# Kernel tuning notes

Hardware: AMD Instinct MI355X
Metric: run time of the kernel (lower is better)

## Reference

```python
import jax, jax.numpy as jnp
import numpy as np

KM_ITERS = 20  # fixed Lloyd iterations (scipy kmeans iterates to tolerance with random init;
               # we use deterministic min/max init so centroid 0 = dark, 1 = bright)


def _kmeans_mask(img2d):
    """2-means clustering of pixel intensities of one [H,W] image + border-vote flip."""
    H, W = img2d.shape
    x = img2d.reshape(-1)  # [N]
    c0 = jnp.stack([x.min(), x.max()])  # deterministic init: centroid0=min, centroid1=max

    def step(c, _):
        code = jnp.argmin(jnp.abs(x[:, None] - c[None, :]), axis=1)  # [N] in {0,1}
        one = code == 1
        n1 = jnp.sum(one)
        n0 = x.shape[0] - n1
        s1 = jnp.sum(jnp.where(one, x, jnp.zeros_like(x)))
        s0 = jnp.sum(x) - s1
        c_new = jnp.stack([s0 / jnp.maximum(n0, 1).astype(x.dtype),
                           s1 / jnp.maximum(n1, 1).astype(x.dtype)])
        return c_new, None

    c, _ = jax.lax.scan(step, c0, None, length=KM_ITERS)
    # final assignment (scipy vq step)
    code = jnp.argmin(jnp.abs(x[:, None] - c[None, :]), axis=1).reshape(H, W)

    # border vote: if >=3 borders are mostly cluster-1, flip so text region is 1
    fc = code[:, 0].sum()
    lc = code[:, -1].sum()
    fr = code[0, :].sum()
    lr = code[-1, :].sum()
    num = ((fr > W // 2).astype(jnp.int32) + (lr > W // 2).astype(jnp.int32)
           + (fc > H // 2).astype(jnp.int32) + (lc > H // 2).astype(jnp.int32))
    mask = jnp.where(num >= 3, 1 - code, code)
    return mask.astype(img2d.dtype)


def get_mask(img_tensor):
    gray = img_tensor.mean(axis=1)  # [B,H,W]
    # clustering is non-differentiable in the original (runs on detached CPU numpy)
    masks = jax.vmap(_kmeans_mask)(jax.lax.stop_gradient(gray))
    return masks[:, None, :, :]  # [B,1,H,W]


def setup_inputs() -> dict:
    key = jax.random.key(0)
    k1, k2 = jax.random.split(key)
    B, C, H, W = 128, 3, 256, 256
    hr_img = jax.random.uniform(k1, (B, C, H, W), dtype=jnp.float32)
    sr_mask = jax.random.uniform(k2, (B, 1, H, W), dtype=jnp.float32)
    return {"hr_img": hr_img, "sr_mask": sr_mask}


def reference(hr_img, sr_mask):
    hr_mask = get_mask(hr_img)  # same spatial size -> no interpolation branch
    return jnp.mean((sr_mask - hr_mask) ** 2)
```

## Files before the change

kernel.cpp:

```cpp
#include <hip/hip_runtime.h>


constexpr int TPB  = 1024;
constexpr int NW   = TPB / 64;
constexpr int NPIX = 65536;
constexpr int VPT  = NPIX / TPB;
constexpr int V4   = VPT / 4;
constexpr int KM_ITERS = 20;

__device__ __forceinline__ float waveSum(float v) {
#pragma unroll
    for (int off = 32; off > 0; off >>= 1) v += __shfl_down(v, off, 64);
    return v;
}
__device__ __forceinline__ float waveMin(float v) {
#pragma unroll
    for (int off = 32; off > 0; off >>= 1) v = fminf(v, __shfl_down(v, off, 64));
    return v;
}
__device__ __forceinline__ float waveMax(float v) {
#pragma unroll
    for (int off = 32; off > 0; off >>= 1) v = fmaxf(v, __shfl_down(v, off, 64));
    return v;
}

__global__ __launch_bounds__(TPB) void kmeans_mask_loss(
        const float* __restrict__ hr, const float* __restrict__ sr,
        float* __restrict__ ws) {
    const int img  = blockIdx.x;
    const int tid  = threadIdx.x;
    const int lane = tid & 63;
    const int wid  = tid >> 6;

    __shared__ float4 sm4[NW];
    __shared__ float  bc[4];

    const float* r = hr + (size_t)img * 3 * NPIX;
    const float* g = r + NPIX;
    const float* b = g + NPIX;

    float v[VPT];
#pragma unroll
    for (int i = 0; i < V4; ++i) {
        const int p = 4 * tid + 4096 * i;
        float4 rr = *(const float4*)(r + p);
        float4 gg = *(const float4*)(g + p);
        float4 bb = *(const float4*)(b + p);
        v[4*i+0] = (rr.x + gg.x + bb.x) * (1.0f / 3.0f);
        v[4*i+1] = (rr.y + gg.y + bb.y) * (1.0f / 3.0f);
        v[4*i+2] = (rr.z + gg.z + bb.z) * (1.0f / 3.0f);
        v[4*i+3] = (rr.w + gg.w + bb.w) * (1.0f / 3.0f);
    }

    float mn = v[0], mx = v[0], sm = 0.0f;
#pragma unroll
    for (int i = 0; i < VPT; ++i) {
        mn = fminf(mn, v[i]); mx = fmaxf(mx, v[i]); sm += v[i];
    }
    mn = waveMin(mn); mx = waveMax(mx); sm = waveSum(sm);
    if (lane == 0) sm4[wid] = make_float4(mn, mx, sm, 0.0f);
    __syncthreads();
    if (wid == 0) {
        float4 x = (lane < NW) ? sm4[lane] : make_float4(3.0e38f, -3.0e38f, 0.0f, 0.0f);
        x.x = waveMin(x.x); x.y = waveMax(x.y); x.z = waveSum(x.z);
        if (lane == 0) { bc[0] = x.x; bc[1] = x.y; bc[2] = x.z; }
    }
    __syncthreads();
    float c0 = bc[0], c1 = bc[1];
    const float S = bc[2];

#pragma unroll 1
    for (int it = 0; it < KM_ITERS; ++it) {
        const float t = 0.5f * (c0 + c1);
        float s1 = 0.0f, n1 = 0.0f;
        if (c1 >= c0) {
#pragma unroll
            for (int i = 0; i < VPT; ++i)
                if (v[i] > t) { s1 += v[i]; n1 += 1.0f; }
        } else {
#pragma unroll
            for (int i = 0; i < VPT; ++i)
                if (v[i] < t) { s1 += v[i]; n1 += 1.0f; }
        }
        s1 = waveSum(s1); n1 = waveSum(n1);
        if (lane == 0) sm4[wid] = make_float4(s1, n1, 0.0f, 0.0f);
        __syncthreads();
        if (wid == 0) {
            float4 x = (lane < NW) ? sm4[lane] : make_float4(0.0f, 0.0f, 0.0f, 0.0f);
            x.x = waveSum(x.x); x.y = waveSum(x.y);
            if (lane == 0) {
                const float S1 = x.x, N1 = x.y;
                bc[1] = S1 / fmaxf(N1, 1.0f);
                bc[0] = (S - S1) / fmaxf((float)NPIX - N1, 1.0f);
            }
        }
        __syncthreads();
        const float nc0 = bc[0], nc1 = bc[1];
        const bool conv = (nc0 == c0) && (nc1 == c1);
        c0 = nc0; c1 = nc1;
        if (conv) break;
    }

    const float t  = 0.5f * (c0 + c1);
    const bool  hi = (c1 >= c0);
    float fc = 0.0f, lc = 0.0f, fr = 0.0f, lr = 0.0f;
#pragma unroll
    for (int i = 0; i < V4; ++i) {
#pragma unroll
        for (int j = 0; j < 4; ++j) {
            const int p   = 4 * tid + 4096 * i + j;
            const int col = p & 255;
            const int row = p >> 8;
            const bool code = hi ? (v[4*i+j] > t) : (v[4*i+j] < t);
            const float cf = code ? 1.0f : 0.0f;
            if (col == 0)   fc += cf;
            if (col == 255) lc += cf;
            if (row == 0)   fr += cf;
            if (row == 255) lr += cf;
        }
    }
    fc = waveSum(fc); lc = waveSum(lc); fr = waveSum(fr); lr = waveSum(lr);
    if (lane == 0) sm4[wid] = make_float4(fc, lc, fr, lr);
    __syncthreads();
    if (wid == 0) {
        float4 x = (lane < NW) ? sm4[lane] : make_float4(0.0f, 0.0f, 0.0f, 0.0f);
        x.x = waveSum(x.x); x.y = waveSum(x.y); x.z = waveSum(x.z); x.w = waveSum(x.w);
        if (lane == 0) {
            const int num = (x.z > 128.0f) + (x.w > 128.0f) +
                            (x.x > 128.0f) + (x.y > 128.0f);
            bc[0] = (num >= 3) ? 1.0f : 0.0f;
        }
    }
    __syncthreads();
    const bool flip = (bc[0] != 0.0f);

    const float* srp = sr + (size_t)img * NPIX;
    float acc = 0.0f;
#pragma unroll
    for (int i = 0; i < V4; ++i) {
        const int p = 4 * tid + 4096 * i;
        float4 s = *(const float4*)(srp + p);
#pragma unroll
        for (int j = 0; j < 4; ++j) {
            const bool code = hi ? (v[4*i+j] > t) : (v[4*i+j] < t);
            const float m = (code != flip) ? 1.0f : 0.0f;
            const float sv = (j == 0) ? s.x : (j == 1) ? s.y : (j == 2) ? s.z : s.w;
            const float d = sv - m;
            acc += d * d;
        }
    }
    acc = waveSum(acc);
    if (lane == 0) sm4[wid] = make_float4(acc, 0.0f, 0.0f, 0.0f);
    __syncthreads();
    if (wid == 0) {
        float x = (lane < NW) ? sm4[lane].x : 0.0f;
        x = waveSum(x);
        if (lane == 0) ws[img] = x;
    }
}

__global__ void finalize_kernel(const float* __restrict__ ws, float* __restrict__ out) {
    const int lane = threadIdx.x;
    float v = ws[lane] + ws[lane + 64];
    v = waveSum(v);
    if (lane == 0) out[0] = v * (1.0f / 8388608.0f);
}

extern "C" void kernel_launch(void* const* d_in, const int* in_sizes, int n_in,
                              void* d_out, int out_size, void* d_ws, size_t ws_size,
                              hipStream_t stream) {
    const float* hr = (const float*)d_in[0];
    const float* sr = (const float*)d_in[1];
    float* out = (float*)d_out;
    float* ws  = (float*)d_ws;

    kmeans_mask_loss<<<128, TPB, 0, stream>>>(hr, sr, ws);
    finalize_kernel<<<1, 64, 0, stream>>>(ws, out);
}
```

Measured before the change: 218.7 us.

## Replace per-pixel Lloyd iterations with histogram prefix-sum k-means across split kernels

The single-block-per-image kernel is replaced by a pipeline. First a 2048-bin per-image histogram of counts and sums is built across 8 blocks per image. One thread then runs the Lloyd iterations against prefix sums, interpolating linearly inside the threshold bin, and separate kernels handle the border vote and the MSE. This removes the 20 passes over register-resident pixels and the low occupancy of 128 blocks. In exchange it re-reads the image twice, adds a memset and five launches, and approximates the threshold-bin split, so centroids and masks can differ from the exact result.

```diff
diff --git a/kernel.cpp b/kernel.cpp
--- a/kernel.cpp
+++ b/kernel.cpp
@@ -1,12 +1,17 @@
 #include <hip/hip_runtime.h>
 
 
-constexpr int TPB  = 1024;
-constexpr int NW   = TPB / 64;
+constexpr int NB   = 2048;
 constexpr int NPIX = 65536;
-constexpr int VPT  = NPIX / TPB;
-constexpr int V4   = VPT / 4;
 constexpr int KM_ITERS = 20;
+
+constexpr size_t OFF_MINENC = 0;
+constexpr size_t OFF_MAXBIT = 512;
+constexpr size_t OFF_TINFO  = 1024;
+constexpr size_t OFF_HCNT   = 4096;
+constexpr size_t OFF_HSUM   = OFF_HCNT + (size_t)128 * NB * 4;
+constexpr size_t OFF_BSUM   = OFF_HSUM + (size_t)128 * NB * 4;
+constexpr size_t MEMSET_BYTES = OFF_BSUM;
 
 __device__ __forceinline__ float waveSum(float v) {
 #pragma unroll
@@ -24,146 +29,227 @@
     return v;
 }
 
-__global__ __launch_bounds__(TPB) void kmeans_mask_loss(
-        const float* __restrict__ hr, const float* __restrict__ sr,
-        float* __restrict__ ws) {
-    const int img  = blockIdx.x;
-    const int tid  = threadIdx.x;
-    const int lane = tid & 63;
-    const int wid  = tid >> 6;
-
-    __shared__ float4 sm4[NW];
-    __shared__ float  bc[4];
+__global__ __launch_bounds__(256) void kA_hist(
+        const float* __restrict__ hr, unsigned* __restrict__ minenc,
+        unsigned* __restrict__ maxbits, unsigned* __restrict__ hcnt,
+        float* __restrict__ hsum) {
+    const int img = blockIdx.x >> 3, part = blockIdx.x & 7, tid = threadIdx.x;
+    const int lane = tid & 63, wid = tid >> 6;
+
+    __shared__ unsigned hcL[NB];
+    __shared__ float    hsL[NB];
+    __shared__ float    smn[4], smx[4];
+    for (int j = tid; j < NB; j += 256) { hcL[j] = 0u; hsL[j] = 0.0f; }
+    __syncthreads();
 
     const float* r = hr + (size_t)img * 3 * NPIX;
     const float* g = r + NPIX;
     const float* b = g + NPIX;
 
-    float v[VPT];
-#pragma unroll
-    for (int i = 0; i < V4; ++i) {
-        const int p = 4 * tid + 4096 * i;
+    float mn = 1e30f, mx = -1e30f;
+#pragma unroll
+    for (int i = 0; i < 8; ++i) {
+        const int p = part * 8192 + i * 1024 + tid * 4;
         float4 rr = *(const float4*)(r + p);
         float4 gg = *(const float4*)(g + p);
         float4 bb = *(const float4*)(b + p);
-        v[4*i+0] = (rr.x + gg.x + bb.x) * (1.0f / 3.0f);
-        v[4*i+1] = (rr.y + gg.y + bb.y) * (1.0f / 3.0f);
-        v[4*i+2] = (rr.z + gg.z + bb.z) * (1.0f / 3.0f);
-        v[4*i+3] = (rr.w + gg.w + bb.w) * (1.0f / 3.0f);
-    }
-
-    float mn = v[0], mx = v[0], sm = 0.0f;
-#pragma unroll
-    for (int i = 0; i < VPT; ++i) {
-        mn = fminf(mn, v[i]); mx = fmaxf(mx, v[i]); sm += v[i];
-    }
-    mn = waveMin(mn); mx = waveMax(mx); sm = waveSum(sm);
-    if (lane == 0) sm4[wid] = make_float4(mn, mx, sm, 0.0f);
-    __syncthreads();
-    if (wid == 0) {
-        float4 x = (lane < NW) ? sm4[lane] : make_float4(3.0e38f, -3.0e38f, 0.0f, 0.0f);
-        x.x = waveMin(x.x); x.y = waveMax(x.y); x.z = waveSum(x.z);
-        if (lane == 0) { bc[0] = x.x; bc[1] = x.y; bc[2] = x.z; }
-    }
-    __syncthreads();
-    float c0 = bc[0], c1 = bc[1];
-    const float S = bc[2];
-
+        float x[4] = { (rr.x + gg.x + bb.x) * (1.0f / 3.0f),
+                       (rr.y + gg.y + bb.y) * (1.0f / 3.0f),
+                       (rr.z + gg.z + bb.z) * (1.0f / 3.0f),
+                       (rr.w + gg.w + bb.w) * (1.0f / 3.0f) };
+#pragma unroll
+        for (int j = 0; j < 4; ++j) {
+            mn = fminf(mn, x[j]); mx = fmaxf(mx, x[j]);
+            int k = (int)(x[j] * (float)NB);
+            k = max(0, min(NB - 1, k));
+            atomicAdd(&hcL[k], 1u);
+            atomicAdd(&hsL[k], x[j]);
+        }
+    }
+    __syncthreads();
+
+    for (int j = tid; j < NB; j += 256) {
+        unsigned c = hcL[j];
+        if (c) {
+            atomicAdd(&hcnt[(size_t)img * NB + j], c);
+            unsafeAtomicAdd(&hsum[(size_t)img * NB + j], hsL[j]);
+        }
+    }
+
+    mn = waveMin(mn); mx = waveMax(mx);
+    if (lane == 0) { smn[wid] = mn; smx[wid] = mx; }
+    __syncthreads();
+    if (tid == 0) {
+        float bmn = fminf(fminf(smn[0], smn[1]), fminf(smn[2], smn[3]));
+        float bmx = fmaxf(fmaxf(smx[0], smx[1]), fmaxf(smx[2], smx[3]));
+        atomicMax(&maxbits[img], __float_as_uint(bmx));
+        atomicMax(&minenc[img], 0xFFFFFFFFu - __float_as_uint(bmn));
+    }
+}
+
+__global__ __launch_bounds__(256) void kB_lloyd(
+        const unsigned* __restrict__ minenc, const unsigned* __restrict__ maxbits,
+        const unsigned* __restrict__ hcnt, const float* __restrict__ hsum,
+        float4* __restrict__ tinfo) {
+    const int img = blockIdx.x, tid = threadIdx.x;
+    __shared__ float sN[NB + 1], sS[NB + 1];
+    __shared__ float tN[256], tS[256];
+
+    const int base = tid * 8;
+    float n8[8], s8[8];
+#pragma unroll
+    for (int u = 0; u < 8; ++u) {
+        n8[u] = (float)hcnt[(size_t)img * NB + base + u];
+        s8[u] = hsum[(size_t)img * NB + base + u];
+    }
+    float accN = 0.0f, accS = 0.0f;
+#pragma unroll
+    for (int u = 7; u >= 0; --u) {
+        accN += n8[u]; n8[u] = accN;
+        accS += s8[u]; s8[u] = accS;
+    }
+    tN[tid] = accN; tS[tid] = accS;
+    __syncthreads();
+    for (int off = 1; off < 256; off <<= 1) {
+        float aN = 0.0f, aS = 0.0f;
+        if (tid + off < 256) { aN = tN[tid + off]; aS = tS[tid + off]; }
+        __syncthreads();
+        tN[tid] += aN; tS[tid] += aS;
+        __syncthreads();
+    }
+    const float exN = (tid < 255) ? tN[tid + 1] : 0.0f;
+    const float exS = (tid < 255) ? tS[tid + 1] : 0.0f;
+#pragma unroll
+    for (int u = 0; u < 8; ++u) { sN[base + u] = n8[u] + exN; sS[base + u] = s8[u] + exS; }
+    if (tid == 0) { sN[NB] = 0.0f; sS[NB] = 0.0f; }
+    __syncthreads();
+
+    if (tid == 0) {
+        const float mn = __uint_as_float(0xFFFFFFFFu - minenc[img]);
+        const float mx = __uint_as_float(maxbits[img]);
+        const float Stot = sS[0];
+        const float Ntot = (float)NPIX;
+        float c0 = mn, c1 = mx;
 #pragma unroll 1
-    for (int it = 0; it < KM_ITERS; ++it) {
-        const float t = 0.5f * (c0 + c1);
-        float s1 = 0.0f, n1 = 0.0f;
-        if (c1 >= c0) {
-#pragma unroll
-            for (int i = 0; i < VPT; ++i)
-                if (v[i] > t) { s1 += v[i]; n1 += 1.0f; }
-        } else {
-#pragma unroll
-            for (int i = 0; i < VPT; ++i)
-                if (v[i] < t) { s1 += v[i]; n1 += 1.0f; }
-        }
-        s1 = waveSum(s1); n1 = waveSum(n1);
-        if (lane == 0) sm4[wid] = make_float4(s1, n1, 0.0f, 0.0f);
-        __syncthreads();
-        if (wid == 0) {
-            float4 x = (lane < NW) ? sm4[lane] : make_float4(0.0f, 0.0f, 0.0f, 0.0f);
-            x.x = waveSum(x.x); x.y = waveSum(x.y);
-            if (lane == 0) {
-                const float S1 = x.x, N1 = x.y;
-                bc[1] = S1 / fmaxf(N1, 1.0f);
-                bc[0] = (S - S1) / fmaxf((float)NPIX - N1, 1.0f);
+        for (int it = 0; it < KM_ITERS; ++it) {
+            const float t = 0.5f * (c0 + c1);
+            float n1, s1;
+            if (c1 == c0) { n1 = 0.0f; s1 = 0.0f; }
+            else {
+                const float f = t * (float)NB;
+                int k = (int)floorf(f);
+                k = max(0, min(NB - 1, k));
+                float frac = (float)(k + 1) - f;
+                frac = fminf(fmaxf(frac, 0.0f), 1.0f);
+                const float cntk = sN[k] - sN[k + 1];
+                const float sumk = sS[k] - sS[k + 1];
+                const float aN = sN[k + 1] + cntk * frac;
+                const float aS = sS[k + 1] + sumk * frac;
+                if (c1 > c0) { n1 = aN; s1 = aS; }
+                else         { n1 = Ntot - aN; s1 = Stot - aS; }
             }
-        }
-        __syncthreads();
-        const float nc0 = bc[0], nc1 = bc[1];
-        const bool conv = (nc0 == c0) && (nc1 == c1);
-        c0 = nc0; c1 = nc1;
-        if (conv) break;
-    }
-
-    const float t  = 0.5f * (c0 + c1);
-    const bool  hi = (c1 >= c0);
-    float fc = 0.0f, lc = 0.0f, fr = 0.0f, lr = 0.0f;
-#pragma unroll
-    for (int i = 0; i < V4; ++i) {
+            const float c1n = s1 / fmaxf(n1, 1.0f);
+            const float c0n = (Stot - s1) / fmaxf(Ntot - n1, 1.0f);
+            if (c1n == c1 && c0n == c0) break;
+            c0 = c0n; c1 = c1n;
+        }
+        float tf, hii;
+        if (c1 == c0) { tf = -1e30f; hii = 0.0f; }
+        else { tf = 0.5f * (c0 + c1); hii = (c1 > c0) ? 1.0f : 0.0f; }
+        tinfo[img] = make_float4(tf, hii, 0.0f, 0.0f);
+    }
+}
+
+__global__ __launch_bounds__(256) void kC_border(
+        const float* __restrict__ hr, float4* __restrict__ tinfo) {
+    const int img = blockIdx.x, tid = threadIdx.x;
+    const int lane = tid & 63, wid = tid >> 6;
+    __shared__ float4 sm[4];
+
+    const float4 ti = tinfo[img];
+    const float t = ti.x;
+    const bool hi = (ti.y != 0.0f);
+
+    const float* r = hr + (size_t)img * 3 * NPIX;
+    const float* g = r + NPIX;
+    const float* b = g + NPIX;
+
+    auto codeAt = [&](int p) -> float {
+        const float x = (r[p] + g[p] + b[p]) * (1.0f / 3.0f);
+        const bool one = hi ? (x > t) : (x < t);
+        return one ? 1.0f : 0.0f;
+    };
+    float fr = codeAt(tid);
+    float lr = codeAt(255 * 256 + tid);
+    float fc = codeAt(tid * 256);
+    float lc = codeAt(tid * 256 + 255);
+
+    fr = waveSum(fr); lr = waveSum(lr); fc = waveSum(fc); lc = waveSum(lc);
+    if (lane == 0) sm[wid] = make_float4(fr, lr, fc, lc);
+    __syncthreads();
+    if (tid == 0) {
+        float FR = sm[0].x + sm[1].x + sm[2].x + sm[3].x;
+        float LR = sm[0].y + sm[1].y + sm[2].y + sm[3].y;
+        float FC = sm[0].z + sm[1].z + sm[2].z + sm[3].z;
+        float LC = sm[0].w + sm[1].w + sm[2].w + sm[3].w;
+        const int num = (FR > 128.0f) + (LR > 128.0f) + (FC > 128.0f) + (LC > 128.0f);
+        tinfo[img].z = (num >= 3) ? 1.0f : 0.0f;
+    }
+}
+
+__global__ __launch_bounds__(256) void kD_mse(
+        const float* __restrict__ hr, const float* __restrict__ sr,
+        const float4* __restrict__ tinfo, float* __restrict__ bsum) {
+    const int img = blockIdx.x >> 3, part = blockIdx.x & 7, tid = threadIdx.x;
+    const int lane = tid & 63, wid = tid >> 6;
+    __shared__ float sm[4];
+
+    const float4 ti = tinfo[img];
+    const float t = ti.x;
+    const bool hi   = (ti.y != 0.0f);
+    const bool flip = (ti.z != 0.0f);
+
+    const float* r = hr + (size_t)img * 3 * NPIX;
+    const float* g = r + NPIX;
+    const float* b = g + NPIX;
+    const float* s = sr + (size_t)img * NPIX;
+
+    float acc = 0.0f;
+#pragma unroll
+    for (int i = 0; i < 8; ++i) {
+        const int p = part * 8192 + i * 1024 + tid * 4;
+        float4 rr = *(const float4*)(r + p);
+        float4 gg = *(const float4*)(g + p);
+        float4 bb = *(const float4*)(b + p);
+        float4 ss = *(const float4*)(s + p);
+        float x[4] = { (rr.x + gg.x + bb.x) * (1.0f / 3.0f),
+                       (rr.y + gg.y + bb.y) * (1.0f / 3.0f),
+                       (rr.z + gg.z + bb.z) * (1.0f / 3.0f),
+                       (rr.w + gg.w + bb.w) * (1.0f / 3.0f) };
+        float sv[4] = { ss.x, ss.y, ss.z, ss.w };
 #pragma unroll
         for (int j = 0; j < 4; ++j) {
-            const int p   = 4 * tid + 4096 * i + j;
-            const int col = p & 255;
-            const int row = p >> 8;
-            const bool code = hi ? (v[4*i+j] > t) : (v[4*i+j] < t);
-            const float cf = code ? 1.0f : 0.0f;
-            if (col == 0)   fc += cf;
-            if (col == 255) lc += cf;
-            if (row == 0)   fr += cf;
-            if (row == 255) lr += cf;
-        }
-    }
-    fc = waveSum(fc); lc = waveSum(lc); fr = waveSum(fr); lr = waveSum(lr);
-    if (lane == 0) sm4[wid] = make_float4(fc, lc, fr, lr);
-    __syncthreads();
-    if (wid == 0) {
-        float4 x = (lane < NW) ? sm4[lane] : make_float4(0.0f, 0.0f, 0.0f, 0.0f);
-        x.x = waveSum(x.x); x.y = waveSum(x.y); x.z = waveSum(x.z); x.w = waveSum(x.w);
-        if (lane == 0) {
-            const int num = (x.z > 128.0f) + (x.w > 128.0f) +
-                            (x.x > 128.0f) + (x.y > 128.0f);
-            bc[0] = (num >= 3) ? 1.0f : 0.0f;
-        }
-    }
-    __syncthreads();
-    const bool flip = (bc[0] != 0.0f);
-
-    const float* srp = sr + (size_t)img * NPIX;
-    float acc = 0.0f;
-#pragma unroll
-    for (int i = 0; i < V4; ++i) {
-        const int p = 4 * tid + 4096 * i;
-        float4 s = *(const float4*)(srp + p);
-#pragma unroll
-        for (int j = 0; j < 4; ++j) {
-            const bool code = hi ? (v[4*i+j] > t) : (v[4*i+j] < t);
-            const float m = (code != flip) ? 1.0f : 0.0f;
-            const float sv = (j == 0) ? s.x : (j == 1) ? s.y : (j == 2) ? s.z : s.w;
-            const float d = sv - m;
+            const bool one = hi ? (x[j] > t) : (x[j] < t);
+            const float m = (one != flip) ? 1.0f : 0.0f;
+            const float d = sv[j] - m;
             acc += d * d;
         }
     }
     acc = waveSum(acc);
-    if (lane == 0) sm4[wid] = make_float4(acc, 0.0f, 0.0f, 0.0f);
-    __syncthreads();
-    if (wid == 0) {
-        float x = (lane < NW) ? sm4[lane].x : 0.0f;
-        x = waveSum(x);
-        if (lane == 0) ws[img] = x;
-    }
-}
-
-__global__ void finalize_kernel(const float* __restrict__ ws, float* __restrict__ out) {
-    const int lane = threadIdx.x;
-    float v = ws[lane] + ws[lane + 64];
+    if (lane == 0) sm[wid] = acc;
+    __syncthreads();
+    if (tid == 0) bsum[blockIdx.x] = sm[0] + sm[1] + sm[2] + sm[3];
+}
+
+__global__ __launch_bounds__(256) void kE_final(
+        const float* __restrict__ bsum, float* __restrict__ out) {
+    const int tid = threadIdx.x, lane = tid & 63, wid = tid >> 6;
+    __shared__ float sm[4];
+    float v = bsum[tid] + bsum[tid + 256] + bsum[tid + 512] + bsum[tid + 768];
     v = waveSum(v);
-    if (lane == 0) out[0] = v * (1.0f / 8388608.0f);
+    if (lane == 0) sm[wid] = v;
+    __syncthreads();
+    if (tid == 0) out[0] = (sm[0] + sm[1] + sm[2] + sm[3]) * (1.0f / 8388608.0f);
 }
 
 extern "C" void kernel_launch(void* const* d_in, const int* in_sizes, int n_in,
@@ -172,8 +258,19 @@
     const float* hr = (const float*)d_in[0];
     const float* sr = (const float*)d_in[1];
     float* out = (float*)d_out;
-    float* ws  = (float*)d_ws;
-
-    kmeans_mask_loss<<<128, TPB, 0, stream>>>(hr, sr, ws);
-    finalize_kernel<<<1, 64, 0, stream>>>(ws, out);
-}
+
+    char* ws = (char*)d_ws;
+    unsigned* minenc  = (unsigned*)(ws + OFF_MINENC);
+    unsigned* maxbits = (unsigned*)(ws + OFF_MAXBIT);
+    float4*   tinfo   = (float4*)(ws + OFF_TINFO);
+    unsigned* hcnt    = (unsigned*)(ws + OFF_HCNT);
+    float*    hsum    = (float*)(ws + OFF_HSUM);
+    float*    bsum    = (float*)(ws + OFF_BSUM);
+
+    hipMemsetAsync(d_ws, 0, MEMSET_BYTES, stream);
+    kA_hist  <<<1024, 256, 0, stream>>>(hr, minenc, maxbits, hcnt, hsum);
+    kB_lloyd <<< 128, 256, 0, stream>>>(minenc, maxbits, hcnt, hsum, tinfo);
+    kC_border<<< 128, 256, 0, stream>>>(hr, tinfo);
+    kD_mse   <<<1024, 256, 0, stream>>>(hr, sr, tinfo, bsum);
+    kE_final <<<   1, 256, 0, stream>>>(bsum, out);
+}
```

New measurement: 209.3 us. -4.3%, faster.

## Replace per-pixel k-means with histogram-based Lloyd iterations across split blocks

Applied to the files above, without the earlier changes.

Splits each image over 8 blocks that quantize gray values to 16 bits and build a 2048-bin shared histogram of counts and sr sums, then a second kernel runs the Lloyd iterations on the histogram. Inside the bin that holds the threshold it assumes pixels are spread uniformly. The loss is computed in closed form from sr sums and squares instead of a second per-pixel pass. This raises parallelism from 128 blocks and removes per-pixel work from the iterations, at the cost of approximating centroids and the mask, which may misclassify pixels near the threshold.

```diff
diff --git a/kernel.cpp b/kernel.cpp
--- a/kernel.cpp
+++ b/kernel.cpp
@@ -1,168 +1,235 @@
 #include <hip/hip_runtime.h>
 
 
-constexpr int TPB  = 1024;
-constexpr int NW   = TPB / 64;
+constexpr int NB   = 2048;
 constexpr int NPIX = 65536;
-constexpr int VPT  = NPIX / TPB;
-constexpr int V4   = VPT / 4;
 constexpr int KM_ITERS = 20;
-
-__device__ __forceinline__ float waveSum(float v) {
+constexpr int TPB  = 256;
+constexpr int BPI  = 8;
+constexpr int GRID_A = 128 * BPI;
+constexpr int PXB  = NPIX / BPI;
+constexpr float QINV = 1.0f / 65536.0f;
+constexpr float BINW = 1.0f / 2048.0f;
+
+constexpr size_t OFF_STATS = 0;
+constexpr size_t OFF_LOSS  = 16384;
+constexpr size_t OFF_SUBC  = 32768;
+constexpr size_t OFF_SUBS  = OFF_SUBC + (size_t)GRID_A * NB * 4;
+
+__device__ __forceinline__ float waveSumF(float v) {
 #pragma unroll
     for (int off = 32; off > 0; off >>= 1) v += __shfl_down(v, off, 64);
     return v;
 }
-__device__ __forceinline__ float waveMin(float v) {
-#pragma unroll
-    for (int off = 32; off > 0; off >>= 1) v = fminf(v, __shfl_down(v, off, 64));
+__device__ __forceinline__ unsigned waveMinU(unsigned v) {
+#pragma unroll
+    for (int off = 32; off > 0; off >>= 1) v = min(v, (unsigned)__shfl_down((int)v, off, 64));
     return v;
 }
-__device__ __forceinline__ float waveMax(float v) {
-#pragma unroll
-    for (int off = 32; off > 0; off >>= 1) v = fmaxf(v, __shfl_down(v, off, 64));
+__device__ __forceinline__ unsigned waveMaxU(unsigned v) {
+#pragma unroll
+    for (int off = 32; off > 0; off >>= 1) v = max(v, (unsigned)__shfl_down((int)v, off, 64));
     return v;
 }
 
-__global__ __launch_bounds__(TPB) void kmeans_mask_loss(
+__global__ __launch_bounds__(TPB) void kA_hist(
         const float* __restrict__ hr, const float* __restrict__ sr,
-        float* __restrict__ ws) {
-    const int img  = blockIdx.x;
-    const int tid  = threadIdx.x;
-    const int lane = tid & 63;
-    const int wid  = tid >> 6;
-
-    __shared__ float4 sm4[NW];
-    __shared__ float  bc[4];
+        float4* __restrict__ stats, unsigned* __restrict__ subc,
+        float* __restrict__ subs) {
+    const int bid = blockIdx.x, tid = threadIdx.x;
+    const int img = bid >> 3, part = bid & 7;
+    const int lane = tid & 63, wid = tid >> 6;
+
+    __shared__ unsigned hc[NB];
+    __shared__ float    hs[NB];
+    __shared__ float4   red[4];
+
+    for (int j = tid; j < NB; j += TPB) { hc[j] = 0u; hs[j] = 0.0f; }
+    __syncthreads();
 
     const float* r = hr + (size_t)img * 3 * NPIX;
     const float* g = r + NPIX;
     const float* b = g + NPIX;
-
-    float v[VPT];
-#pragma unroll
-    for (int i = 0; i < V4; ++i) {
-        const int p = 4 * tid + 4096 * i;
+    const float* sp = sr + (size_t)img * NPIX;
+
+    unsigned umn = 65535u, umx = 0u;
+    float s1 = 0.0f, s2 = 0.0f;
+#pragma unroll
+    for (int i = 0; i < 8; ++i) {
+        const int p = part * PXB + i * 1024 + tid * 4;
         float4 rr = *(const float4*)(r + p);
         float4 gg = *(const float4*)(g + p);
         float4 bb = *(const float4*)(b + p);
-        v[4*i+0] = (rr.x + gg.x + bb.x) * (1.0f / 3.0f);
-        v[4*i+1] = (rr.y + gg.y + bb.y) * (1.0f / 3.0f);
-        v[4*i+2] = (rr.z + gg.z + bb.z) * (1.0f / 3.0f);
-        v[4*i+3] = (rr.w + gg.w + bb.w) * (1.0f / 3.0f);
-    }
-
-    float mn = v[0], mx = v[0], sm = 0.0f;
-#pragma unroll
-    for (int i = 0; i < VPT; ++i) {
-        mn = fminf(mn, v[i]); mx = fmaxf(mx, v[i]); sm += v[i];
-    }
-    mn = waveMin(mn); mx = waveMax(mx); sm = waveSum(sm);
-    if (lane == 0) sm4[wid] = make_float4(mn, mx, sm, 0.0f);
-    __syncthreads();
-    if (wid == 0) {
-        float4 x = (lane < NW) ? sm4[lane] : make_float4(3.0e38f, -3.0e38f, 0.0f, 0.0f);
-        x.x = waveMin(x.x); x.y = waveMax(x.y); x.z = waveSum(x.z);
-        if (lane == 0) { bc[0] = x.x; bc[1] = x.y; bc[2] = x.z; }
-    }
-    __syncthreads();
-    float c0 = bc[0], c1 = bc[1];
-    const float S = bc[2];
+        float4 ss = *(const float4*)(sp + p);
+        float x[4] = { (rr.x + gg.x + bb.x) * (1.0f / 3.0f),
+                       (rr.y + gg.y + bb.y) * (1.0f / 3.0f),
+                       (rr.z + gg.z + bb.z) * (1.0f / 3.0f),
+                       (rr.w + gg.w + bb.w) * (1.0f / 3.0f) };
+        const float sv[4] = { ss.x, ss.y, ss.z, ss.w };
+#pragma unroll
+        for (int j = 0; j < 4; ++j) {
+            unsigned uu = (unsigned)(x[j] * 65536.0f);
+            uu = min(uu, 65535u);
+            umn = min(umn, uu); umx = max(umx, uu);
+            atomicAdd(&hc[uu >> 5], 1u);
+            atomicAdd(&hs[uu >> 5], sv[j]);
+            s1 += sv[j];
+            s2 += sv[j] * sv[j];
+        }
+    }
+    __syncthreads();
+
+    unsigned* oc = subc + (size_t)bid * NB;
+    float*    os = subs + (size_t)bid * NB;
+    for (int j = tid; j < NB; j += TPB) { oc[j] = hc[j]; os[j] = hs[j]; }
+
+    umn = waveMinU(umn); umx = waveMaxU(umx);
+    s1 = waveSumF(s1);   s2 = waveSumF(s2);
+    if (lane == 0) red[wid] = make_float4((float)umn, (float)umx, s1, s2);
+    __syncthreads();
+    if (tid == 0) {
+        stats[bid] = make_float4(
+            fminf(fminf(red[0].x, red[1].x), fminf(red[2].x, red[3].x)),
+            fmaxf(fmaxf(red[0].y, red[1].y), fmaxf(red[2].y, red[3].y)),
+            red[0].z + red[1].z + red[2].z + red[3].z,
+            red[0].w + red[1].w + red[2].w + red[3].w);
+    }
+}
+
+__global__ __launch_bounds__(TPB) void kB_solve(
+        const float* __restrict__ hr, const float4* __restrict__ stats,
+        const unsigned* __restrict__ subc, const float* __restrict__ subs,
+        float* __restrict__ loss) {
+    const int img = blockIdx.x, tid = threadIdx.x;
+    const int lane = tid & 63, wid = tid >> 6;
+    __shared__ float w1[4], w2[4];
+    __shared__ float4 w4[4];
+
+    const int base = tid * 8;
+    float n8[8], t8[8], c8[8];
+#pragma unroll
+    for (int u = 0; u < 8; ++u) {
+        const int j = base + u;
+        unsigned c = 0; float s = 0.0f;
+#pragma unroll
+        for (int q = 0; q < BPI; ++q) {
+            c += subc[(size_t)(img * BPI + q) * NB + j];
+            s += subs[(size_t)(img * BPI + q) * NB + j];
+        }
+        n8[u] = (float)c;
+        t8[u] = s;
+        c8[u] = ((float)j + 0.484375f) * BINW;
+    }
+    float imn = 65535.0f, imx = 0.0f, Ss = 0.0f, Sq = 0.0f;
+#pragma unroll
+    for (int q = 0; q < BPI; ++q) {
+        const float4 st = stats[img * BPI + q];
+        imn = fminf(imn, st.x); imx = fmaxf(imx, st.y);
+        Ss += st.z; Sq += st.w;
+    }
+    float pS = 0.0f;
+#pragma unroll
+    for (int u = 0; u < 8; ++u) pS += n8[u] * c8[u];
+    pS = waveSumF(pS);
+    if (lane == 0) w1[wid] = pS;
+    __syncthreads();
+    const float Stot = w1[0] + w1[1] + w1[2] + w1[3];
+    const float Ntot = (float)NPIX;
+    float c0 = imn * QINV, c1 = imx * QINV;
+    __syncthreads();
 
 #pragma unroll 1
     for (int it = 0; it < KM_ITERS; ++it) {
         const float t = 0.5f * (c0 + c1);
-        float s1 = 0.0f, n1 = 0.0f;
-        if (c1 >= c0) {
-#pragma unroll
-            for (int i = 0; i < VPT; ++i)
-                if (v[i] > t) { s1 += v[i]; n1 += 1.0f; }
-        } else {
-#pragma unroll
-            for (int i = 0; i < VPT; ++i)
-                if (v[i] < t) { s1 += v[i]; n1 += 1.0f; }
-        }
-        s1 = waveSum(s1); n1 = waveSum(n1);
-        if (lane == 0) sm4[wid] = make_float4(s1, n1, 0.0f, 0.0f);
+        float aN = 0.0f, aS = 0.0f;
+        if (c1 != c0) {
+#pragma unroll
+            for (int u = 0; u < 8; ++u) {
+                const float bs = (float)(base + u) * BINW, be = bs + BINW;
+                if (t <= bs) { aN += n8[u]; aS += n8[u] * c8[u]; }
+                else if (t < be) {
+                    const float fr = (be - t) * (float)NB;
+                    aN += n8[u] * fr;
+                    aS += n8[u] * fr * 0.5f * (t + be);
+                }
+            }
+        }
+        aN = waveSumF(aN); aS = waveSumF(aS);
+        if (lane == 0) { w1[wid] = aN; w2[wid] = aS; }
         __syncthreads();
-        if (wid == 0) {
-            float4 x = (lane < NW) ? sm4[lane] : make_float4(0.0f, 0.0f, 0.0f, 0.0f);
-            x.x = waveSum(x.x); x.y = waveSum(x.y);
-            if (lane == 0) {
-                const float S1 = x.x, N1 = x.y;
-                bc[1] = S1 / fmaxf(N1, 1.0f);
-                bc[0] = (S - S1) / fmaxf((float)NPIX - N1, 1.0f);
-            }
-        }
+        const float AN = w1[0] + w1[1] + w1[2] + w1[3];
+        const float AS = w2[0] + w2[1] + w2[2] + w2[3];
+        float n1, s1;
+        if (c1 == c0)     { n1 = 0.0f;       s1 = 0.0f; }
+        else if (c1 > c0) { n1 = AN;         s1 = AS; }
+        else              { n1 = Ntot - AN;  s1 = Stot - AS; }
+        const float c1n = s1 / fmaxf(n1, 1.0f);
+        const float c0n = (Stot - s1) / fmaxf(Ntot - n1, 1.0f);
         __syncthreads();
-        const float nc0 = bc[0], nc1 = bc[1];
-        const bool conv = (nc0 == c0) && (nc1 == c1);
-        c0 = nc0; c1 = nc1;
-        if (conv) break;
-    }
-
-    const float t  = 0.5f * (c0 + c1);
-    const bool  hi = (c1 >= c0);
-    float fc = 0.0f, lc = 0.0f, fr = 0.0f, lr = 0.0f;
-#pragma unroll
-    for (int i = 0; i < V4; ++i) {
-#pragma unroll
-        for (int j = 0; j < 4; ++j) {
-            const int p   = 4 * tid + 4096 * i + j;
-            const int col = p & 255;
-            const int row = p >> 8;
-            const bool code = hi ? (v[4*i+j] > t) : (v[4*i+j] < t);
-            const float cf = code ? 1.0f : 0.0f;
-            if (col == 0)   fc += cf;
-            if (col == 255) lc += cf;
-            if (row == 0)   fr += cf;
-            if (row == 255) lr += cf;
-        }
-    }
-    fc = waveSum(fc); lc = waveSum(lc); fr = waveSum(fr); lr = waveSum(lr);
-    if (lane == 0) sm4[wid] = make_float4(fc, lc, fr, lr);
-    __syncthreads();
-    if (wid == 0) {
-        float4 x = (lane < NW) ? sm4[lane] : make_float4(0.0f, 0.0f, 0.0f, 0.0f);
-        x.x = waveSum(x.x); x.y = waveSum(x.y); x.z = waveSum(x.z); x.w = waveSum(x.w);
-        if (lane == 0) {
-            const int num = (x.z > 128.0f) + (x.w > 128.0f) +
-                            (x.x > 128.0f) + (x.y > 128.0f);
-            bc[0] = (num >= 3) ? 1.0f : 0.0f;
-        }
-    }
-    __syncthreads();
-    const bool flip = (bc[0] != 0.0f);
-
-    const float* srp = sr + (size_t)img * NPIX;
-    float acc = 0.0f;
-#pragma unroll
-    for (int i = 0; i < V4; ++i) {
-        const int p = 4 * tid + 4096 * i;
-        float4 s = *(const float4*)(srp + p);
-#pragma unroll
-        for (int j = 0; j < 4; ++j) {
-            const bool code = hi ? (v[4*i+j] > t) : (v[4*i+j] < t);
-            const float m = (code != flip) ? 1.0f : 0.0f;
-            const float sv = (j == 0) ? s.x : (j == 1) ? s.y : (j == 2) ? s.z : s.w;
-            const float d = sv - m;
-            acc += d * d;
-        }
-    }
-    acc = waveSum(acc);
-    if (lane == 0) sm4[wid] = make_float4(acc, 0.0f, 0.0f, 0.0f);
-    __syncthreads();
-    if (wid == 0) {
-        float x = (lane < NW) ? sm4[lane].x : 0.0f;
-        x = waveSum(x);
-        if (lane == 0) ws[img] = x;
-    }
-}
-
-__global__ void finalize_kernel(const float* __restrict__ ws, float* __restrict__ out) {
+        if (c1n == c1 && c0n == c0) break;
+        c0 = c0n; c1 = c1n;
+    }
+    const bool degen = (c1 == c0);
+    const float t  = degen ? -1e30f : 0.5f * (c0 + c1);
+    const bool hi  = (!degen) && (c1 > c0);
+
+    float aN = 0.0f, aT = 0.0f;
+#pragma unroll
+    for (int u = 0; u < 8; ++u) {
+        const float bs = (float)(base + u) * BINW, be = bs + BINW;
+        if (t <= bs) { aN += n8[u]; aT += t8[u]; }
+        else if (t < be) {
+            const float fr = (be - t) * (float)NB;
+            aN += n8[u] * fr;
+            aT += t8[u] * fr;
+        }
+    }
+    aN = waveSumF(aN); aT = waveSumF(aT);
+    if (lane == 0) { w1[wid] = aN; w2[wid] = aT; }
+
+    const float* r = hr + (size_t)img * 3 * NPIX;
+    const float* g = r + NPIX;
+    const float* b = g + NPIX;
+    auto codeAt = [&](int p) -> float {
+        const float x = (r[p] + g[p] + b[p]) * (1.0f / 3.0f);
+        const unsigned uu = min((unsigned)(x * 65536.0f), 65535u);
+        const float xq = (float)uu * QINV;
+        const bool one = hi ? (xq > t) : (xq < t);
+        return one ? 1.0f : 0.0f;
+    };
+    float frq = codeAt(tid);
+    float lrq = codeAt(255 * 256 + tid);
+    float fcq = codeAt(tid * 256);
+    float lcq = codeAt(tid * 256 + 255);
+    __syncthreads();
+    const float AN = w1[0] + w1[1] + w1[2] + w1[3];
+    const float AT = w2[0] + w2[1] + w2[2] + w2[3];
+    frq = waveSumF(frq); lrq = waveSumF(lrq);
+    fcq = waveSumF(fcq); lcq = waveSumF(lcq);
+    if (lane == 0) w4[wid] = make_float4(frq, lrq, fcq, lcq);
+    __syncthreads();
+    if (tid == 0) {
+        const float FR = w4[0].x + w4[1].x + w4[2].x + w4[3].x;
+        const float LR = w4[0].y + w4[1].y + w4[2].y + w4[3].y;
+        const float FC = w4[0].z + w4[1].z + w4[2].z + w4[3].z;
+        const float LC = w4[0].w + w4[1].w + w4[2].w + w4[3].w;
+        const int num = (FR > 128.0f) + (LR > 128.0f) +
+                        (FC > 128.0f) + (LC > 128.0f);
+        const bool flip = (num >= 3);
+        float N1, S1;
+        if (degen)   { N1 = 0.0f;        S1 = 0.0f; }
+        else if (hi) { N1 = AN;          S1 = AT; }
+        else         { N1 = Ntot - AN;   S1 = Ss - AT; }
+        const float mse0 = Sq - 2.0f * S1 + N1;
+        const float mse1 = Sq - 2.0f * (Ss - S1) + (Ntot - N1);
+        loss[img] = flip ? mse1 : mse0;
+    }
+}
+
+__global__ void kD_final(const float* __restrict__ loss, float* __restrict__ out) {
     const int lane = threadIdx.x;
-    float v = ws[lane] + ws[lane + 64];
-    v = waveSum(v);
+    float v = loss[lane] + loss[lane + 64];
+    v = waveSumF(v);
     if (lane == 0) out[0] = v * (1.0f / 8388608.0f);
 }
 
@@ -172,8 +239,14 @@
     const float* hr = (const float*)d_in[0];
     const float* sr = (const float*)d_in[1];
     float* out = (float*)d_out;
-    float* ws  = (float*)d_ws;
-
-    kmeans_mask_loss<<<128, TPB, 0, stream>>>(hr, sr, ws);
-    finalize_kernel<<<1, 64, 0, stream>>>(ws, out);
-}
+
+    char* ws = (char*)d_ws;
+    float4*   stats = (float4*)(ws + OFF_STATS);
+    float*    loss  = (float*)(ws + OFF_LOSS);
+    unsigned* subc  = (unsigned*)(ws + OFF_SUBC);
+    float*    subs  = (float*)(ws + OFF_SUBS);
+
+    kA_hist <<<GRID_A, TPB, 0, stream>>>(hr, sr, stats, subc, subs);
+    kB_solve<<<128,    TPB, 0, stream>>>(hr, stats, subc, subs, loss);
+    kD_final<<<1,      64,  0, stream>>>(loss, out);
+}
```

Result: faster. 204.7 us (-6.4%).
